# Optimization experiments

Hardware: AMD Instinct MI355X
Metric: run time of the kernel (lower is better)

The kernel has to match this reference:

```python
import jax, jax.numpy as jnp
import numpy as np

EPS = 1e-5  # BatchNorm eps (inference-style with running stats)


def setup_inputs() -> dict:
    key = jax.random.key(0)
    ks = jax.random.split(key, 8)
    b, ci, co, K, ca, H, W = 32, 64, 64, 4, 16, 128, 128
    r = lambda k, s, sc=1.0: jax.random.normal(k, s, dtype=jnp.float32) * sc
    return {
        "x": r(ks[0], (b, ci, H, W)),
        "prep_w": r(ks[1], (ca, ci), 0.1),
        "bn_gamma": jnp.ones((ca,), jnp.float32),
        "bn_beta": jnp.zeros((ca,), jnp.float32),
        "bn_mean": jnp.zeros((ca,), jnp.float32),
        "bn_var": jnp.ones((ca,), jnp.float32),
        "fc_sp_w": r(ks[2], (9, ca), 0.1),
        "fc_sp_b": jnp.zeros((9,), jnp.float32),
        "fc_ch_w": r(ks[3], (ci, ca), 0.1),
        "fc_ch_b": jnp.zeros((ci,), jnp.float32),
        "fc_f_w": r(ks[4], (co, ca), 0.1),
        "fc_f_b": jnp.zeros((co,), jnp.float32),
        "fc_k_w": r(ks[5], (K, ca), 0.1),
        "fc_k_b": jnp.zeros((K,), jnp.float32),
        "kernels": r(ks[6], (K, co, ci, 3, 3), 0.1),
    }


def reference(x, prep_w, bn_gamma, bn_beta, bn_mean, bn_var,
              fc_sp_w, fc_sp_b, fc_ch_w, fc_ch_b, fc_f_w, fc_f_b,
              fc_k_w, fc_k_b, kernels):
    b, ci, h, w = x.shape
    K, co = kernels.shape[0], kernels.shape[1]
    # attention trunk: global avg pool -> 1x1 conv -> BN -> ReLU
    pooled = x.mean(axis=(2, 3))                              # (b, ci)
    att = pooled @ prep_w.T                                   # (b, ca)
    att = (att - bn_mean) * jax.lax.rsqrt(bn_var + EPS) * bn_gamma + bn_beta
    att = jax.nn.relu(att)
    # four attention heads
    sp = jax.nn.sigmoid(att @ fc_sp_w.T + fc_sp_b).reshape(b, 1, 1, 1, 3, 3)
    cha = jax.nn.sigmoid(att @ fc_ch_w.T + fc_ch_b)           # (b, ci)
    fa = jax.nn.sigmoid(att @ fc_f_w.T + fc_f_b)              # (b, co)
    ka = jax.nn.softmax(att @ fc_k_w.T + fc_k_b, axis=1).reshape(b, K, 1, 1, 1, 1)
    # per-sample dynamic weight synthesis: sum over kernel_num
    wdyn = jnp.sum(sp * ka * kernels[None], axis=1)           # (b, co, ci, 3, 3)
    # grouped conv with groups = batch
    xm = (x * cha[:, :, None, None]).reshape(1, b * ci, h, w)
    wg = wdyn.reshape(b * co, ci, 3, 3)
    out = jax.lax.conv_general_dilated(
        xm, wg, window_strides=(1, 1), padding=[(1, 1), (1, 1)],
        dimension_numbers=("NCHW", "OIHW", "NCHW"), feature_group_count=b)
    out = out.reshape(b, co, h, w)
    return out * fa[:, :, None, None]
```

## Files before the change

kernel.cpp:

```cpp
#include <hip/hip_runtime.h>
#include <math.h>

#define NB 32
#define CI 64
#define CO 64
#define CA 16
#define NK 4
#define HH 128
#define WW 128
#define EPSBN 1e-5f

typedef __bf16 bf16x8 __attribute__((ext_vector_type(8)));
typedef float f32x4 __attribute__((ext_vector_type(4)));

__device__ inline unsigned short f2bf(float f) {
    union { float f; unsigned u; } c; c.f = f;
    return (unsigned short)((c.u + 0x7fffu + ((c.u >> 16) & 1u)) >> 16);
}

__device__ inline unsigned cvt_pk_bf16(float lo, float hi) {
    unsigned r;
    asm("v_cvt_pk_bf16_f32 %0, %1, %2" : "=v"(r) : "v"(lo), "v"(hi));
    return r;
}

__device__ inline void gload_lds16(const void* g, void* l) {
    __builtin_amdgcn_global_load_lds(
        (const __attribute__((address_space(1))) unsigned int*)g,
        (__attribute__((address_space(3))) unsigned int*)l, 16, 0, 0);
}

#define WS_ZERO   0
#define WS_POOLED 64
#define WS_CHA    2112
#define WS_FA     4160
#define WS_KA     6208
#define WS_SP     6336
#define WS_W2T    8192

__global__ __launch_bounds__(256, 4) void pool_kernel(const float* __restrict__ x,
                                                      float* __restrict__ pooled,
                                                      float* __restrict__ zeros) {
    if (blockIdx.x == 0 && threadIdx.x < 64) zeros[threadIdx.x] = 0.f;
    const int plane = blockIdx.x;
    const float4* p = (const float4*)(x + (size_t)plane * (HH * WW));
    float4 v[16];
    #pragma unroll
    for (int i = 0; i < 16; ++i) v[i] = p[threadIdx.x + 256 * i];
    float s = 0.f;
    #pragma unroll
    for (int i = 0; i < 16; ++i) s += v[i].x + v[i].y + v[i].z + v[i].w;
    #pragma unroll
    for (int off = 32; off > 0; off >>= 1) s += __shfl_down(s, off);
    __shared__ float red[4];
    if ((threadIdx.x & 63) == 0) red[threadIdx.x >> 6] = s;
    __syncthreads();
    if (threadIdx.x == 0)
        pooled[plane] = red[0] + red[1] + red[2] + red[3];
}

__global__ __launch_bounds__(512) void attn3(
    const float* __restrict__ pooled, const float* __restrict__ prep_w,
    const float* __restrict__ bn_g, const float* __restrict__ bn_b,
    const float* __restrict__ bn_m, const float* __restrict__ bn_v,
    const float* __restrict__ fc_sp_w, const float* __restrict__ fc_sp_b,
    const float* __restrict__ fc_ch_w, const float* __restrict__ fc_ch_b,
    const float* __restrict__ fc_f_w,  const float* __restrict__ fc_f_b,
    const float* __restrict__ fc_k_w,  const float* __restrict__ fc_k_b,
    float* __restrict__ sp, float* __restrict__ cha,
    float* __restrict__ fa, float* __restrict__ ka) {
    __shared__ float pooled_s[NB * CI];
    __shared__ float att_s[NB * CA];
    const int tid = threadIdx.x;
    const float scale = 1.f / (HH * WW);
    #pragma unroll
    for (int i = 0; i < 4; ++i) {
        const int e = tid + 512 * i;
        pooled_s[e] = pooled[e];
    }
    __syncthreads();
    const int b = tid >> 4, a = tid & 15;
    {
        float s = 0.f;
        const float* pv = pooled_s + b * CI;
        #pragma unroll
        for (int c = 0; c < CI; ++c) s += pv[c] * prep_w[a * CI + c];
        s = (s * scale - bn_m[a]) * rsqrtf(bn_v[a] + EPSBN) * bn_g[a] + bn_b[a];
        att_s[b * CA + a] = fmaxf(s, 0.f);
    }
    __syncthreads();
    float av[CA];
    #pragma unroll
    for (int i = 0; i < CA; ++i) av[i] = att_s[b * CA + i];

    const int j = a;
    if (j < 9) {
        float s = fc_sp_b[j];
        #pragma unroll
        for (int i = 0; i < CA; ++i) s += av[i] * fc_sp_w[j * CA + i];
        sp[b * 9 + j] = 1.f / (1.f + expf(-s));
    }
    #pragma unroll
    for (int t = 0; t < 4; ++t) {
        const int c = j * 4 + t;
        float s1 = fc_ch_b[c], s2 = fc_f_b[c];
        #pragma unroll
        for (int i = 0; i < CA; ++i) {
            s1 += av[i] * fc_ch_w[c * CA + i];
            s2 += av[i] * fc_f_w[c * CA + i];
        }
        cha[b * CI + c] = 1.f / (1.f + expf(-s1));
        fa[b * CO + c]  = 1.f / (1.f + expf(-s2));
    }
    if (j == 0) {
        float kv[NK], m = -1e30f;
        #pragma unroll
        for (int k = 0; k < NK; ++k) {
            float s = fc_k_b[k];
            #pragma unroll
            for (int i = 0; i < CA; ++i) s += av[i] * fc_k_w[k * CA + i];
            kv[k] = s; m = fmaxf(m, s);
        }
        float den = 0.f;
        #pragma unroll
        for (int k = 0; k < NK; ++k) { kv[k] = expf(kv[k] - m); den += kv[k]; }
        #pragma unroll
        for (int k = 0; k < NK; ++k) ka[b * NK + k] = kv[k] / den;
    }
}

__global__ __launch_bounds__(256) void w2t2(const float* __restrict__ kernels,
                                            const float* __restrict__ sp,
                                            const float* __restrict__ cha,
                                            const float* __restrict__ fa,
                                            const float* __restrict__ ka,
                                            unsigned short* __restrict__ w2t) {
    const int bid = blockIdx.x;
    const int b  = bid >> 4;
    const int o  = (bid & 15) * 4 + (threadIdx.x >> 6);
    const int i  = threadIdx.x & 63;
    float kw[NK][9];
    #pragma unroll
    for (int k = 0; k < NK; ++k) {
        const float* kp = kernels + ((size_t)(k * CO + o) * CI + i) * 9;
        #pragma unroll
        for (int t = 0; t < 9; ++t) kw[k][t] = kp[t];
    }
    float kav[NK];
    #pragma unroll
    for (int k = 0; k < NK; ++k) kav[k] = ka[b * NK + k];
    const float base = cha[b * CI + i] * fa[b * CO + o];
    #pragma unroll
    for (int tap = 0; tap < 9; ++tap) {
        float s = 0.f;
        #pragma unroll
        for (int k = 0; k < NK; ++k) s += kav[k] * kw[k][tap];
        w2t[((size_t)(b * 9 + tap) * CO + o) * CI + i] = f2bf(s * sp[b * 9 + tap] * base);
    }
}

#define ABASE 26624
#define ABUFB 12288

__global__ __launch_bounds__(256, 3) void conv_fused(const float* __restrict__ x,
                                                     const unsigned short* __restrict__ w2t,
                                                     const float* __restrict__ zeros,
                                                     float* __restrict__ out) {
    __shared__ __align__(16) unsigned char xs[ABASE + 2 * ABUFB];
    const int tid  = threadIdx.x;
    const int lane = tid & 63;
    const int wv   = tid >> 6;
    const int orig = blockIdx.x;
    const int bid  = (orig & 7) * 512 + (orig >> 3);
    const int b    = bid >> 7;
    const int rem  = bid & 127;
    const int colg = rem & 3;
    const int hg   = rem >> 2;
    const int h0 = hg * 4;
    const int w0 = colg * 32;

    const unsigned short* w2base = w2t + (size_t)b * 36864;

    auto stageA = [&](int c) {
        const int ks = c / 3, v = c - ks * 3;
        unsigned char* abuf = xs + ABASE + (c & 1) * ABUFB;
        for (int ch = wv; ch < 12; ch += 4) {
            const int u  = ch >> 2;
            const int q  = ch & 3;
            const unsigned short* g = w2base + (size_t)(u * 3 + v) * 4096
                                    + lane * 64 + ks * 32 + q * 8;
            gload_lds16(g, abuf + (ch << 10));
        }
    };

    const int qlane = lane & 3;
    const int g     = lane >> 2;
    float4 La[9], Lb[9];
    #pragma unroll
    for (int it = 0; it < 9; ++it) {
        const int base = (wv * 9 + it) * 16;
        const int blk  = base >> 5;
        const int row  = blk / 3;
        const int iq   = blk - row * 3;
        const int cip  = (base & 31) + g;
        const int hh   = h0 - 1 + row;
        const int cg   = w0 - 8 + iq * 16 + qlane * 4;
        const bool ok  = ((unsigned)hh < (unsigned)HH) && ((unsigned)cg <= 124u);
        const float* p0 = x + ((size_t)(b * CI + 2 * cip) * HH + hh) * WW + cg;
        const float* pa = ok ? p0 : zeros;
        const float* pb = ok ? (p0 + HH * WW) : zeros;
        La[it] = *(const float4*)pa;
        Lb[it] = *(const float4*)pb;
    }
    stageA(0);

    #pragma unroll
    for (int it = 0; it < 9; ++it) {
        const int base = (wv * 9 + it) * 16;
        const int blk  = base >> 5;
        const int row  = blk / 3;
        const int iq   = blk - row * 3;
        const int cip  = (base & 31) + g;
        unsigned char* rbase = xs + row * 4352;
        const int oct = cip >> 2, lo = (cip & 3) * 4;
        const float av[4] = {La[it].x, La[it].y, La[it].z, La[it].w};
        const float cv[4] = {Lb[it].x, Lb[it].y, Lb[it].z, Lb[it].w};
        #pragma unroll
        for (int e = 0; e < 4; ++e) {
            const int cl_ = iq * 16 + qlane * 4 + e - 7;
            if ((unsigned)cl_ < 34u) {
                *(unsigned*)(rbase + cl_ * 128 + ((oct ^ (cl_ & 7)) << 4) + lo) =
                    cvt_pk_bf16(av[e], cv[e]);
            }
        }
    }
    __syncthreads();

    const int cl = lane & 15;
    const int kq = lane >> 4;
    const int cohalf = wv & 1;
    const int colh   = wv >> 1;

    f32x4 acc[2][4];
    #pragma unroll
    for (int og = 0; og < 2; ++og)
        #pragma unroll
        for (int t = 0; t < 4; ++t)
            #pragma unroll
            for (int e = 0; e < 4; ++e) acc[og][t][e] = 0.f;

    const int lcol0 = colh * 16 + cl;
    const int aoff  = kq * 1024 + (cohalf * 32 + cl) * 16;

    #pragma unroll
    for (int c = 0; c < 6; ++c) {
        const int ks = c / 3, v = c - ks * 3;
        if (c < 5) stageA(c + 1);
        const unsigned char* abuf = xs + ABASE + (c & 1) * ABUFB;
        const int lcol = lcol0 + v;
        const int sw = ((ks << 2) + kq) ^ (lcol & 7);
        const unsigned char* bp = xs + (((lcol << 3) + sw) << 4);
        bf16x8 Bf[6];
        #pragma unroll
        for (int r = 0; r < 6; ++r) Bf[r] = *(const bf16x8*)(bp + r * 4352);
        __builtin_amdgcn_s_setprio(1);
        #pragma unroll
        for (int u = 0; u < 3; ++u) {
            const unsigned char* ap = abuf + u * 4096 + aoff;
            const bf16x8 A0 = *(const bf16x8*)(ap);
            const bf16x8 A1 = *(const bf16x8*)(ap + 256);
            #pragma unroll
            for (int t = 0; t < 4; ++t)
                acc[0][t] = __builtin_amdgcn_mfma_f32_16x16x32_bf16(A0, Bf[t + u], acc[0][t], 0, 0, 0);
            #pragma unroll
            for (int t = 0; t < 4; ++t)
                acc[1][t] = __builtin_amdgcn_mfma_f32_16x16x32_bf16(A1, Bf[t + u], acc[1][t], 0, 0, 0);
        }
        __builtin_amdgcn_s_setprio(0);
        if (c < 5) __syncthreads();
    }

    #pragma unroll
    for (int og = 0; og < 2; ++og)
        #pragma unroll
        for (int t = 0; t < 4; ++t) {
            float* op = out + ((size_t)(b * CO + cohalf * 32 + og * 16 + kq * 4) * HH + h0 + t) * WW
                      + w0 + colh * 16 + cl;
            #pragma unroll
            for (int rg = 0; rg < 4; ++rg)
                op[(size_t)rg * (HH * WW)] = acc[og][t][rg];
        }
}

extern "C" void kernel_launch(void* const* d_in, const int* in_sizes, int n_in,
                              void* d_out, int out_size, void* d_ws, size_t ws_size,
                              hipStream_t stream) {
    const float* x        = (const float*)d_in[0];
    const float* prep_w   = (const float*)d_in[1];
    const float* bn_g     = (const float*)d_in[2];
    const float* bn_b     = (const float*)d_in[3];
    const float* bn_m     = (const float*)d_in[4];
    const float* bn_v     = (const float*)d_in[5];
    const float* fc_sp_w  = (const float*)d_in[6];
    const float* fc_sp_b  = (const float*)d_in[7];
    const float* fc_ch_w  = (const float*)d_in[8];
    const float* fc_ch_b  = (const float*)d_in[9];
    const float* fc_f_w   = (const float*)d_in[10];
    const float* fc_f_b   = (const float*)d_in[11];
    const float* fc_k_w   = (const float*)d_in[12];
    const float* fc_k_b   = (const float*)d_in[13];
    const float* kernels  = (const float*)d_in[14];
    float* out = (float*)d_out;
    float* ws  = (float*)d_ws;

    float* zeros  = ws + WS_ZERO;
    float* pooled = ws + WS_POOLED;
    float* cha    = ws + WS_CHA;
    float* fa     = ws + WS_FA;
    float* ka     = ws + WS_KA;
    float* sp     = ws + WS_SP;
    unsigned short* w2t = (unsigned short*)(ws + WS_W2T);

    pool_kernel<<<NB * CI, 256, 0, stream>>>(x, pooled, zeros);
    attn3<<<1, 512, 0, stream>>>(pooled, prep_w, bn_g, bn_b, bn_m, bn_v,
                                 fc_sp_w, fc_sp_b, fc_ch_w, fc_ch_b,
                                 fc_f_w, fc_f_b, fc_k_w, fc_k_b,
                                 sp, cha, fa, ka);
    w2t2<<<NB * 16, 256, 0, stream>>>(kernels, sp, cha, fa, ka, w2t);
    conv_fused<<<4096, 256, 0, stream>>>(x, w2t, zeros, out);
}
```

Before: 116.9 us.

## Fuse attention heads into weight synthesis and register-stage conv weight tiles

The single-block attention kernel is removed. Each weight-synthesis block now recomputes the attention trunk and heads for its own sample, using shuffles to share the 16 attention values across lanes, so one launch and a serial single-block stage disappear. In exchange the small attention matmuls are computed redundantly by every block. The conv kernel also replaces its direct global-to-LDS weight loads with register prefetch two chunks ahead and an LDS write after each chunk's MFMAs, aiming to hide load latency at the cost of more registers.

```diff
diff --git a/kernel.cpp b/kernel.cpp
--- a/kernel.cpp
+++ b/kernel.cpp
@@ -32,10 +32,6 @@
 
 #define WS_ZERO   0
 #define WS_POOLED 64
-#define WS_CHA    2112
-#define WS_FA     4160
-#define WS_KA     6208
-#define WS_SP     6336
 #define WS_W2T    8192
 
 __global__ __launch_bounds__(256, 4) void pool_kernel(const float* __restrict__ x,
@@ -59,103 +55,90 @@
         pooled[plane] = red[0] + red[1] + red[2] + red[3];
 }
 
-__global__ __launch_bounds__(512) void attn3(
-    const float* __restrict__ pooled, const float* __restrict__ prep_w,
+__global__ __launch_bounds__(256) void w2t3(
+    const float* __restrict__ kernels, const float* __restrict__ pooled,
+    const float* __restrict__ prep_w,
     const float* __restrict__ bn_g, const float* __restrict__ bn_b,
     const float* __restrict__ bn_m, const float* __restrict__ bn_v,
     const float* __restrict__ fc_sp_w, const float* __restrict__ fc_sp_b,
     const float* __restrict__ fc_ch_w, const float* __restrict__ fc_ch_b,
     const float* __restrict__ fc_f_w,  const float* __restrict__ fc_f_b,
     const float* __restrict__ fc_k_w,  const float* __restrict__ fc_k_b,
-    float* __restrict__ sp, float* __restrict__ cha,
-    float* __restrict__ fa, float* __restrict__ ka) {
-    __shared__ float pooled_s[NB * CI];
-    __shared__ float att_s[NB * CA];
-    const int tid = threadIdx.x;
+    unsigned short* __restrict__ w2t) {
+    const int bid = blockIdx.x;
+    const int b  = bid >> 4;
+    const int wv = threadIdx.x >> 6;
+    const int o  = (bid & 15) * 4 + wv;
+    const int lane = threadIdx.x & 63;
+    const int i  = lane;
     const float scale = 1.f / (HH * WW);
-    #pragma unroll
-    for (int i = 0; i < 4; ++i) {
-        const int e = tid + 512 * i;
-        pooled_s[e] = pooled[e];
-    }
-    __syncthreads();
-    const int b = tid >> 4, a = tid & 15;
+
+    float kw[NK][9];
+    #pragma unroll
+    for (int k = 0; k < NK; ++k) {
+        const float* kp = kernels + ((size_t)(k * CO + o) * CI + i) * 9;
+        #pragma unroll
+        for (int t = 0; t < 9; ++t) kw[k][t] = kp[t];
+    }
+
+    const int a_ = lane & 15;
+    float att;
     {
         float s = 0.f;
-        const float* pv = pooled_s + b * CI;
-        #pragma unroll
-        for (int c = 0; c < CI; ++c) s += pv[c] * prep_w[a * CI + c];
-        s = (s * scale - bn_m[a]) * rsqrtf(bn_v[a] + EPSBN) * bn_g[a] + bn_b[a];
-        att_s[b * CA + a] = fmaxf(s, 0.f);
-    }
-    __syncthreads();
+        const float* pv = pooled + b * CI;
+        const float* wv_ = prep_w + a_ * CI;
+        #pragma unroll
+        for (int c = 0; c < CI; ++c) s += pv[c] * wv_[c];
+        s = (s * scale - bn_m[a_]) * rsqrtf(bn_v[a_] + EPSBN) * bn_g[a_] + bn_b[a_];
+        att = fmaxf(s, 0.f);
+    }
     float av[CA];
     #pragma unroll
-    for (int i = 0; i < CA; ++i) av[i] = att_s[b * CA + i];
-
-    const int j = a;
-    if (j < 9) {
-        float s = fc_sp_b[j];
-        #pragma unroll
-        for (int i = 0; i < CA; ++i) s += av[i] * fc_sp_w[j * CA + i];
-        sp[b * 9 + j] = 1.f / (1.f + expf(-s));
-    }
-    #pragma unroll
-    for (int t = 0; t < 4; ++t) {
-        const int c = j * 4 + t;
-        float s1 = fc_ch_b[c], s2 = fc_f_b[c];
-        #pragma unroll
-        for (int i = 0; i < CA; ++i) {
-            s1 += av[i] * fc_ch_w[c * CA + i];
-            s2 += av[i] * fc_f_w[c * CA + i];
-        }
-        cha[b * CI + c] = 1.f / (1.f + expf(-s1));
-        fa[b * CO + c]  = 1.f / (1.f + expf(-s2));
-    }
-    if (j == 0) {
+    for (int k = 0; k < CA; ++k) av[k] = __shfl(att, (lane & 48) + k);
+
+    float cha_i, fa_o;
+    {
+        float s1 = fc_ch_b[i], s2 = fc_f_b[o];
+        #pragma unroll
+        for (int k = 0; k < CA; ++k) {
+            s1 += av[k] * fc_ch_w[i * CA + k];
+            s2 += av[k] * fc_f_w[o * CA + k];
+        }
+        cha_i = 1.f / (1.f + expf(-s1));
+        fa_o  = 1.f / (1.f + expf(-s2));
+    }
+    float kav[NK];
+    {
         float kv[NK], m = -1e30f;
         #pragma unroll
         for (int k = 0; k < NK; ++k) {
             float s = fc_k_b[k];
             #pragma unroll
-            for (int i = 0; i < CA; ++i) s += av[i] * fc_k_w[k * CA + i];
+            for (int t = 0; t < CA; ++t) s += av[t] * fc_k_w[k * CA + t];
             kv[k] = s; m = fmaxf(m, s);
         }
         float den = 0.f;
         #pragma unroll
         for (int k = 0; k < NK; ++k) { kv[k] = expf(kv[k] - m); den += kv[k]; }
         #pragma unroll
-        for (int k = 0; k < NK; ++k) ka[b * NK + k] = kv[k] / den;
-    }
-}
-
-__global__ __launch_bounds__(256) void w2t2(const float* __restrict__ kernels,
-                                            const float* __restrict__ sp,
-                                            const float* __restrict__ cha,
-                                            const float* __restrict__ fa,
-                                            const float* __restrict__ ka,
-                                            unsigned short* __restrict__ w2t) {
-    const int bid = blockIdx.x;
-    const int b  = bid >> 4;
-    const int o  = (bid & 15) * 4 + (threadIdx.x >> 6);
-    const int i  = threadIdx.x & 63;
-    float kw[NK][9];
-    #pragma unroll
-    for (int k = 0; k < NK; ++k) {
-        const float* kp = kernels + ((size_t)(k * CO + o) * CI + i) * 9;
-        #pragma unroll
-        for (int t = 0; t < 9; ++t) kw[k][t] = kp[t];
-    }
-    float kav[NK];
-    #pragma unroll
-    for (int k = 0; k < NK; ++k) kav[k] = ka[b * NK + k];
-    const float base = cha[b * CI + i] * fa[b * CO + o];
+        for (int k = 0; k < NK; ++k) kav[k] = kv[k] / den;
+    }
+    float spv[9];
+    #pragma unroll
+    for (int t = 0; t < 9; ++t) {
+        float s = fc_sp_b[t];
+        #pragma unroll
+        for (int k = 0; k < CA; ++k) s += av[k] * fc_sp_w[t * CA + k];
+        spv[t] = 1.f / (1.f + expf(-s));
+    }
+
+    const float base = cha_i * fa_o;
     #pragma unroll
     for (int tap = 0; tap < 9; ++tap) {
         float s = 0.f;
         #pragma unroll
         for (int k = 0; k < NK; ++k) s += kav[k] * kw[k][tap];
-        w2t[((size_t)(b * 9 + tap) * CO + o) * CI + i] = f2bf(s * sp[b * 9 + tap] * base);
+        w2t[((size_t)(b * 9 + tap) * CO + o) * CI + i] = f2bf(s * spv[tap] * base);
     }
 }
 
@@ -181,17 +164,28 @@
 
     const unsigned short* w2base = w2t + (size_t)b * 36864;
 
-    auto stageA = [&](int c) {
+    const int aq = tid >> 6, ao = tid & 63;
+    uint4 Areg[2][3];
+    auto AloadReg = [&](int c) {
         const int ks = c / 3, v = c - ks * 3;
+        #pragma unroll
+        for (int j = 0; j < 3; ++j)
+            Areg[c & 1][j] = *(const uint4*)(w2base + (size_t)(j * 3 + v) * 4096
+                                             + ao * 64 + ks * 32 + aq * 8);
+    };
+    auto AwriteLds = [&](int c) {
         unsigned char* abuf = xs + ABASE + (c & 1) * ABUFB;
+        #pragma unroll
+        for (int j = 0; j < 3; ++j)
+            *(uint4*)(abuf + j * 4096 + aq * 1024 + ao * 16) = Areg[c & 1][j];
+    };
+    {
         for (int ch = wv; ch < 12; ch += 4) {
-            const int u  = ch >> 2;
-            const int q  = ch & 3;
-            const unsigned short* g = w2base + (size_t)(u * 3 + v) * 4096
-                                    + lane * 64 + ks * 32 + q * 8;
-            gload_lds16(g, abuf + (ch << 10));
-        }
-    };
+            const int u = ch >> 2, q = ch & 3;
+            gload_lds16(w2base + (size_t)(u * 3 + 0) * 4096 + lane * 64 + q * 8,
+                        xs + ABASE + (ch << 10));
+        }
+    }
 
     const int qlane = lane & 3;
     const int g     = lane >> 2;
@@ -212,7 +206,7 @@
         La[it] = *(const float4*)pa;
         Lb[it] = *(const float4*)pb;
     }
-    stageA(0);
+    AloadReg(1);
 
     #pragma unroll
     for (int it = 0; it < 9; ++it) {
@@ -255,7 +249,7 @@
     #pragma unroll
     for (int c = 0; c < 6; ++c) {
         const int ks = c / 3, v = c - ks * 3;
-        if (c < 5) stageA(c + 1);
+        if (c < 4) AloadReg(c + 2);
         const unsigned char* abuf = xs + ABASE + (c & 1) * ABUFB;
         const int lcol = lcol0 + v;
         const int sw = ((ks << 2) + kq) ^ (lcol & 7);
@@ -277,7 +271,10 @@
                 acc[1][t] = __builtin_amdgcn_mfma_f32_16x16x32_bf16(A1, Bf[t + u], acc[1][t], 0, 0, 0);
         }
         __builtin_amdgcn_s_setprio(0);
-        if (c < 5) __syncthreads();
+        if (c < 5) {
+            AwriteLds(c + 1);
+            __syncthreads();
+        }
     }
 
     #pragma unroll
@@ -315,17 +312,12 @@
 
     float* zeros  = ws + WS_ZERO;
     float* pooled = ws + WS_POOLED;
-    float* cha    = ws + WS_CHA;
-    float* fa     = ws + WS_FA;
-    float* ka     = ws + WS_KA;
-    float* sp     = ws + WS_SP;
     unsigned short* w2t = (unsigned short*)(ws + WS_W2T);
 
     pool_kernel<<<NB * CI, 256, 0, stream>>>(x, pooled, zeros);
-    attn3<<<1, 512, 0, stream>>>(pooled, prep_w, bn_g, bn_b, bn_m, bn_v,
-                                 fc_sp_w, fc_sp_b, fc_ch_w, fc_ch_b,
-                                 fc_f_w, fc_f_b, fc_k_w, fc_k_b,
-                                 sp, cha, fa, ka);
-    w2t2<<<NB * 16, 256, 0, stream>>>(kernels, sp, cha, fa, ka, w2t);
+    w2t3<<<NB * 16, 256, 0, stream>>>(kernels, pooled, prep_w,
+                                      bn_g, bn_b, bn_m, bn_v,
+                                      fc_sp_w, fc_sp_b, fc_ch_w, fc_ch_b,
+                                      fc_f_w, fc_f_b, fc_k_w, fc_k_b, w2t);
     conv_fused<<<4096, 256, 0, stream>>>(x, w2t, zeros, out);
 }
```

New measurement: 160.2 us. +37.1%, slower.
